# Kernel tuning notes

Measured on AMD Instinct MI355X. Metric: run time of the kernel, lower is better.

The kernel has to match this reference:

```python
import jax, jax.numpy as jnp
import numpy as np

D_MODEL = 1024
D_STATE = 16
D_CONV = 4
EXPAND = 2
HEADDIM = 8
D_INNER = EXPAND * D_MODEL            # 2048
NHEADS = D_INNER // HEADDIM           # 256
CONV_DIM = D_INNER + 2 * D_STATE      # 2080 (ngroups=1)
D_IN_PROJ = 2 * D_INNER + 2 * D_STATE + NHEADS  # 4384
B_SZ, SEQ = 4, 2048
EPS = 1e-5


def setup_inputs() -> dict:
    key = jax.random.key(0)
    ks = jax.random.split(key, 8)
    return {
        "x": jax.random.normal(ks[0], (B_SZ, SEQ, D_MODEL), jnp.float32),
        "ln_w": jnp.ones((D_MODEL,), jnp.float32),
        "ln_b": jnp.zeros((D_MODEL,), jnp.float32),
        "W_in": jax.random.normal(ks[1], (D_MODEL, D_IN_PROJ), jnp.float32) * 0.02,
        "conv_w": jax.random.normal(ks[2], (D_CONV, 1, CONV_DIM), jnp.float32) * 0.2,
        "conv_b": jnp.zeros((CONV_DIM,), jnp.float32),
        "A_log": jnp.log(jax.random.uniform(ks[3], (NHEADS,), jnp.float32, 1.0, 16.0)),
        "Dp": jnp.ones((NHEADS,), jnp.float32) + 0.1 * jax.random.normal(ks[4], (NHEADS,), jnp.float32),
        "dt_bias": 0.5 * jax.random.normal(ks[5], (NHEADS,), jnp.float32),
        "rms_w": jnp.ones((D_INNER,), jnp.float32),
        "W_out": jax.random.normal(ks[6], (D_INNER, D_MODEL), jnp.float32) * 0.02,
    }


def _mamba_block(x, ln_w, ln_b, W_in, conv_w, conv_b, A_log, Dp, dt_bias, rms_w, W_out):
    B, L, _ = x.shape
    # pre-norm LayerNorm
    mu = jnp.mean(x, axis=-1, keepdims=True)
    var = jnp.mean((x - mu) ** 2, axis=-1, keepdims=True)
    xn = (x - mu) * jax.lax.rsqrt(var + EPS) * ln_w + ln_b

    # in_proj -> z, xBC, dt
    u = xn @ W_in                                    # (B, L, 4384)
    z = u[..., :D_INNER]
    xBC = u[..., D_INNER:D_INNER + CONV_DIM]
    dt = jax.nn.softplus(u[..., -NHEADS:] + dt_bias)  # (B, L, NHEADS)

    # causal depthwise conv1d + SiLU
    xp = jnp.pad(xBC, ((0, 0), (D_CONV - 1, 0), (0, 0)))
    xBC = jax.lax.conv_general_dilated(
        xp, conv_w, window_strides=(1,), padding="VALID",
        dimension_numbers=("NWC", "WIO", "NWC"), feature_group_count=CONV_DIM)
    xBC = jax.nn.silu(xBC + conv_b)

    xs = xBC[..., :D_INNER].reshape(B, L, NHEADS, HEADDIM)   # SSM input
    Bm = xBC[..., D_INNER:D_INNER + D_STATE]                  # (B, L, N)
    Cm = xBC[..., D_INNER + D_STATE:]                          # (B, L, N)

    A = -jnp.exp(A_log)                                       # (NHEADS,)

    def step(h, inp):
        # h: (B, H, P, N)
        x_t, B_t, C_t, dt_t = inp
        dA = jnp.exp(dt_t * A)                                 # (B, H)
        h = h * dA[..., None, None] + jnp.einsum("bh,bhp,bn->bhpn", dt_t, x_t, B_t)
        y = jnp.einsum("bhpn,bn->bhp", h, C_t)
        return h, y

    h0 = jnp.zeros((B, NHEADS, HEADDIM, D_STATE), x.dtype)
    _, ys = jax.lax.scan(step, h0, (xs.swapaxes(0, 1), Bm.swapaxes(0, 1),
                                     Cm.swapaxes(0, 1), dt.swapaxes(0, 1)))
    y = ys.swapaxes(0, 1) + Dp[None, None, :, None] * xs       # (B, L, H, P)
    y = y.reshape(B, L, D_INNER)

    # gated RMSNorm: rmsnorm(y * silu(z)) * weight
    g = y * jax.nn.silu(z)
    g = g * jax.lax.rsqrt(jnp.mean(g * g, axis=-1, keepdims=True) + EPS) * rms_w

    return x + g @ W_out


def reference(x, ln_w, ln_b, W_in, conv_w, conv_b, A_log, Dp, dt_bias, rms_w, W_out):
    return _mamba_block(x, ln_w, ln_b, W_in, conv_w, conv_b, A_log, Dp, dt_bias, rms_w, W_out)
```

## Files before the change

### kernel.cpp

```cpp
#include <hip/hip_runtime.h>

typedef __bf16 bf16;
typedef __attribute__((ext_vector_type(8))) __bf16 bf16x8;
typedef __attribute__((ext_vector_type(4))) float f32x4;

#define B_SZ 4
#define SEQ 2048
#define DM 1024
#define DIN 2048
#define NH 256
#define DSTATE 16
#define CONVD 2080
#define DPROJ 4384
#define NPAD1 4608
#define MROWS 8192
#define NC 64
#define LC 32
#define UROWB 8768

__device__ __forceinline__ void gload_lds16(const void* g, void* l) {
  __builtin_amdgcn_global_load_lds(
      (__attribute__((address_space(1))) void*)g,
      (__attribute__((address_space(3))) void*)l, 16, 0, 0);
}

template <int N>
__device__ __forceinline__ void vm_wait() {
  asm volatile("s_waitcnt vmcnt(%0)" ::"n"(N) : "memory");
}
__device__ __forceinline__ void bar() { asm volatile("s_barrier" ::: "memory"); }
__device__ __forceinline__ void lgkm0() {
  asm volatile("s_waitcnt lgkmcnt(0)" ::: "memory");
}

__global__ void transpose_cvt(const float* __restrict__ W, bf16* __restrict__ WT,
                              int K, int N, int Npad) {
  __shared__ float tile[32][33];
  int k0 = blockIdx.x * 32, n0 = blockIdx.y * 32;
  int tx = threadIdx.x, ty = threadIdx.y;
#pragma unroll
  for (int j = 0; j < 4; j++) {
    int k = k0 + ty + 8 * j, n = n0 + tx;
    tile[ty + 8 * j][tx] = (k < K && n < N) ? W[(size_t)k * N + n] : 0.f;
  }
  __syncthreads();
#pragma unroll
  for (int j = 0; j < 4; j++) {
    int n = n0 + ty + 8 * j, k = k0 + tx;
    if (n < Npad && k < K) WT[(size_t)n * K + k] = (bf16)tile[tx][ty + 8 * j];
  }
}

__global__ __launch_bounds__(256) void ln_kernel(const float* __restrict__ x,
                                                 const float* __restrict__ lw,
                                                 const float* __restrict__ lb,
                                                 bf16* __restrict__ xn) {
  int row = blockIdx.x;
  int t = threadIdx.x;
  f32x4 v4 = ((const f32x4*)(x + (size_t)row * DM))[t];
  float v0 = v4[0], v1 = v4[1], v2 = v4[2], v3 = v4[3];
  float s = v0 + v1 + v2 + v3;
  float s2 = v0 * v0 + v1 * v1 + v2 * v2 + v3 * v3;
#pragma unroll
  for (int off = 32; off > 0; off >>= 1) {
    s += __shfl_down(s, off);
    s2 += __shfl_down(s2, off);
  }
  __shared__ float ps[8];
  int wave = t >> 6, lane = t & 63;
  if (lane == 0) { ps[wave] = s; ps[4 + wave] = s2; }
  __syncthreads();
  s = ps[0] + ps[1] + ps[2] + ps[3];
  s2 = ps[4] + ps[5] + ps[6] + ps[7];
  float mean = s * (1.f / DM);
  float var = s2 * (1.f / DM) - mean * mean;
  float rstd = rsqrtf(var + 1e-5f);
  f32x4 wv = ((const f32x4*)lw)[t];
  f32x4 bv = ((const f32x4*)lb)[t];
  bf16 o[4];
  o[0] = (bf16)((v0 - mean) * rstd * wv[0] + bv[0]);
  o[1] = (bf16)((v1 - mean) * rstd * wv[1] + bv[1]);
  o[2] = (bf16)((v2 - mean) * rstd * wv[2] + bv[2]);
  o[3] = (bf16)((v3 - mean) * rstd * wv[3] + bv[3]);
  bf16* dst = xn + (size_t)row * DM + t * 4;
  dst[0] = o[0]; dst[1] = o[1]; dst[2] = o[2]; dst[3] = o[3];
}

__global__ __launch_bounds__(512, 2) void gemm1_8p(const bf16* __restrict__ A,
                                                   const bf16* __restrict__ BT,
                                                   bf16* __restrict__ C) {
  __shared__ char lds[139264];
  int bid = blockIdx.x;
  int xcd = bid & 7;
  int l = bid >> 3;
  int bm = xcd * 4 + ((l >> 3) & 3);
  int bn = (l >> 5) * 8 + (l & 7);
  int m0 = bm * 256, n0 = bn * 192;
  int t = threadIdx.x, lane = t & 63, wave = t >> 6;
  int wm = wave >> 2, wn = wave & 3;
  int lr16 = lane & 15, kq = lane >> 4;
  int ts0 = kq ^ (lr16 & 7);
  int ts1 = (4 + kq) ^ (lr16 & 7);
  int sw = (lane & 7) ^ (lane >> 3);
  int l8 = lane >> 3;
  const char* Ab = (const char*)A;
  const char* Bb = (const char*)BT;

  auto stA = [&](int kt) {
    char* slot = lds + (kt & 1) * 32768;
    size_t ko = (size_t)kt * 128 + sw * 16;
#pragma unroll
    for (int g = 0; g < 4; g++) {
      int c = wave * 4 + g;
      gload_lds16(Ab + (size_t)(m0 + c * 8 + l8) * 2048 + ko, slot + c * 1024);
    }
  };
  auto stB = [&](int kt) {
    char* slot = lds + 65536 + (kt % 3) * 24576;
    size_t ko = (size_t)kt * 128 + sw * 16;
#pragma unroll
    for (int g = 0; g < 3; g++) {
      int c = wave * 3 + g;
      gload_lds16(Bb + (size_t)(n0 + c * 8 + l8) * 2048 + ko, slot + c * 1024);
    }
  };

  f32x4 acc[8][3] = {};
  bf16x8 a_[4][2], b_[3][2];

  stA(0); stB(0); stA(1); stB(1);
  vm_wait<7>();
  bar();
#pragma unroll 1
  for (int kt = 0; kt < 16; kt++) {
    {
      const char* sa = lds + (kt & 1) * 32768;
      const char* sb = lds + 65536 + (kt % 3) * 24576;
#pragma unroll
      for (int mi = 0; mi < 4; mi++) {
        int lrow = wm * 128 + mi * 16 + lr16;
        a_[mi][0] = *(const bf16x8*)(sa + lrow * 128 + ts0 * 16);
        a_[mi][1] = *(const bf16x8*)(sa + lrow * 128 + ts1 * 16);
      }
#pragma unroll
      for (int ni = 0; ni < 3; ni++) {
        int lrow = wn * 48 + ni * 16 + lr16;
        b_[ni][0] = *(const bf16x8*)(sb + lrow * 128 + ts0 * 16);
        b_[ni][1] = *(const bf16x8*)(sb + lrow * 128 + ts1 * 16);
      }
      if (kt >= 1 && kt < 15) stA(kt + 1);
      if (kt < 14) stB(kt + 2);
      bar();
      lgkm0();
      __builtin_amdgcn_s_setprio(1);
#pragma unroll
      for (int mi = 0; mi < 4; mi++)
#pragma unroll
        for (int ni = 0; ni < 3; ni++) {
          acc[mi][ni] = __builtin_amdgcn_mfma_f32_16x16x32_bf16(a_[mi][0], b_[ni][0], acc[mi][ni], 0, 0, 0);
          acc[mi][ni] = __builtin_amdgcn_mfma_f32_16x16x32_bf16(a_[mi][1], b_[ni][1], acc[mi][ni], 0, 0, 0);
        }
      __builtin_amdgcn_s_setprio(0);
      bar();
    }
    {
      const char* sa = lds + (kt & 1) * 32768;
#pragma unroll
      for (int mi = 0; mi < 4; mi++) {
        int lrow = wm * 128 + 64 + mi * 16 + lr16;
        a_[mi][0] = *(const bf16x8*)(sa + lrow * 128 + ts0 * 16);
        a_[mi][1] = *(const bf16x8*)(sa + lrow * 128 + ts1 * 16);
      }
      if (kt <= 13) vm_wait<3>();
      else if (kt == 14) vm_wait<0>();
      bar();
      lgkm0();
      __builtin_amdgcn_s_setprio(1);
#pragma unroll
      for (int mi = 0; mi < 4; mi++)
#pragma unroll
        for (int ni = 0; ni < 3; ni++) {
          acc[4 + mi][ni] = __builtin_amdgcn_mfma_f32_16x16x32_bf16(a_[mi][0], b_[ni][0], acc[4 + mi][ni], 0, 0, 0);
          acc[4 + mi][ni] = __builtin_amdgcn_mfma_f32_16x16x32_bf16(a_[mi][1], b_[ni][1], acc[4 + mi][ni], 0, 0, 0);
        }
      __builtin_amdgcn_s_setprio(0);
      bar();
    }
  }
#pragma unroll
  for (int fr = 0; fr < 8; fr++)
#pragma unroll
    for (int ni = 0; ni < 3; ni++) {
      int row = m0 + wm * 128 + fr * 16 + kq * 4;
      int col = n0 + wn * 48 + ni * 16 + lr16;
      f32x4 v = acc[fr][ni];
      if (col < 4384) {
#pragma unroll
        for (int r = 0; r < 4; r++)
          C[(size_t)(row + r) * DPROJ + col] = (bf16)v[r];
      }
    }
}

__global__ __launch_bounds__(512, 2) void gemm2_8p(const bf16* __restrict__ A,
                                                   const bf16* __restrict__ BT,
                                                   float* __restrict__ C,
                                                   const float* __restrict__ Xres) {
  __shared__ char lds[147456];
  int bid = blockIdx.x;
  int swz = (bid & 7) * 32 + (bid >> 3);
  int bm = swz >> 2, bn = swz & 3;
  int m0 = bm * 128, n0 = bn * 256;
  int t = threadIdx.x, lane = t & 63, wave = t >> 6;
  int wm = wave >> 2, wn = wave & 3;
  int lr16 = lane & 15, kq = lane >> 4;
  int ts0 = kq ^ (lr16 & 7);
  int ts1 = (4 + kq) ^ (lr16 & 7);
  int sw = (lane & 7) ^ (lane >> 3);
  int l8 = lane >> 3;
  const char* Ab = (const char*)A;
  const char* Bb = (const char*)BT;

  auto stA = [&](int kt) {
    char* slot = lds + (kt % 3) * 16384;
    size_t ko = (size_t)kt * 128 + sw * 16;
#pragma unroll
    for (int g = 0; g < 2; g++) {
      int c = wave * 2 + g;
      gload_lds16(Ab + (size_t)(m0 + c * 8 + l8) * 4096 + ko, slot + c * 1024);
    }
  };
  auto stB = [&](int kt) {
    char* slot = lds + 49152 + (kt % 3) * 32768;
    size_t ko = (size_t)kt * 128 + sw * 16;
#pragma unroll
    for (int g = 0; g < 4; g++) {
      int c = wave * 4 + g;
      gload_lds16(Bb + (size_t)(n0 + c * 8 + l8) * 4096 + ko, slot + c * 1024);
    }
  };

  f32x4 acc[4][4] = {};
  bf16x8 a_[4][2], b_[2][2];

  stA(0); stB(0); stA(1); stB(1);
  vm_wait<6>();
  bar();
#pragma unroll 1
  for (int kt = 0; kt < 32; kt++) {
    const char* sa = lds + (kt % 3) * 16384;
    const char* sb = lds + 49152 + (kt % 3) * 32768;
    {
#pragma unroll
      for (int mi = 0; mi < 4; mi++) {
        int lrow = wm * 64 + mi * 16 + lr16;
        a_[mi][0] = *(const bf16x8*)(sa + lrow * 128 + ts0 * 16);
        a_[mi][1] = *(const bf16x8*)(sa + lrow * 128 + ts1 * 16);
      }
#pragma unroll
      for (int ni = 0; ni < 2; ni++) {
        int lrow = wn * 64 + ni * 16 + lr16;
        b_[ni][0] = *(const bf16x8*)(sb + lrow * 128 + ts0 * 16);
        b_[ni][1] = *(const bf16x8*)(sb + lrow * 128 + ts1 * 16);
      }
      if (kt + 2 < 32) { stA(kt + 2); stB(kt + 2); }
      bar();
      lgkm0();
      __builtin_amdgcn_s_setprio(1);
#pragma unroll
      for (int mi = 0; mi < 4; mi++)
#pragma unroll
        for (int ni = 0; ni < 2; ni++) {
          acc[mi][ni] = __builtin_amdgcn_mfma_f32_16x16x32_bf16(a_[mi][0], b_[ni][0], acc[mi][ni], 0, 0, 0);
          acc[mi][ni] = __builtin_amdgcn_mfma_f32_16x16x32_bf16(a_[mi][1], b_[ni][1], acc[mi][ni], 0, 0, 0);
        }
      __builtin_amdgcn_s_setprio(0);
      bar();
    }
    {
#pragma unroll
      for (int ni = 0; ni < 2; ni++) {
        int lrow = wn * 64 + (2 + ni) * 16 + lr16;
        b_[ni][0] = *(const bf16x8*)(sb + lrow * 128 + ts0 * 16);
        b_[ni][1] = *(const bf16x8*)(sb + lrow * 128 + ts1 * 16);
      }
      if (kt <= 29) vm_wait<6>();
      else if (kt == 30) vm_wait<0>();
      bar();
      lgkm0();
      __builtin_amdgcn_s_setprio(1);
#pragma unroll
      for (int mi = 0; mi < 4; mi++)
#pragma unroll
        for (int ni = 0; ni < 2; ni++) {
          acc[mi][2 + ni] = __builtin_amdgcn_mfma_f32_16x16x32_bf16(a_[mi][0], b_[ni][0], acc[mi][2 + ni], 0, 0, 0);
          acc[mi][2 + ni] = __builtin_amdgcn_mfma_f32_16x16x32_bf16(a_[mi][1], b_[ni][1], acc[mi][2 + ni], 0, 0, 0);
        }
      __builtin_amdgcn_s_setprio(0);
      bar();
    }
  }
#pragma unroll
  for (int mi = 0; mi < 4; mi++)
#pragma unroll
    for (int ni = 0; ni < 4; ni++) {
      int row = m0 + wm * 64 + mi * 16 + kq * 4;
      int col = n0 + wn * 64 + ni * 16 + lr16;
      f32x4 v = acc[mi][ni];
#pragma unroll
      for (int r = 0; r < 4; r++) {
        size_t o = (size_t)(row + r) * DM + col;
        C[o] = Xres[o] + v[r];
      }
    }
}

__global__ __launch_bounds__(256) void conv_prep3(const bf16* __restrict__ u,
                                                  const float* __restrict__ cw,
                                                  const float* __restrict__ cb,
                                                  const float* __restrict__ dt_bias,
                                                  bf16* __restrict__ xs,
                                                  float* __restrict__ BC,
                                                  float* __restrict__ dtf) {
  const int JPR = 292;
  int idx = blockIdx.x * 256 + threadIdx.x;
  if (idx >= MROWS * JPR) return;
  int row = idx / JPR;
  int j = idx - row * JPR;
  int t = row & (SEQ - 1);
  if (j < 260) {
    int c0 = j * 8;
    float acc[8];
#pragma unroll
    for (int i = 0; i < 8; i++) acc[i] = cb[c0 + i];
    const bf16* ub = u + (size_t)row * DPROJ + DIN + c0;
#pragma unroll
    for (int tap = 0; tap < 4; tap++) {
      int tt = t - 3 + tap;
      if (tt >= 0) {
        bf16x8 uv = *(const bf16x8*)(ub + (ptrdiff_t)(tap - 3) * DPROJ);
        const float* wv = cw + tap * CONVD + c0;
#pragma unroll
        for (int i = 0; i < 8; i++) acc[i] += wv[i] * (float)uv[i];
      }
    }
    if (c0 < DIN) {
      bf16x8 o;
#pragma unroll
      for (int i = 0; i < 8; i++) {
        float sv = acc[i] / (1.f + __expf(-acc[i]));
        o[i] = (bf16)sv;
      }
      *(bf16x8*)(xs + (size_t)row * DIN + c0) = o;
    } else {
      float* bc = BC + (size_t)row * 32 + (c0 - DIN);
#pragma unroll
      for (int i = 0; i < 8; i++) bc[i] = acc[i] / (1.f + __expf(-acc[i]));
    }
  } else {
    int h0 = (j - 260) * 8;
    bf16x8 uv = *(const bf16x8*)(u + (size_t)row * DPROJ + (DPROJ - NH) + h0);
    float* dst = dtf + (size_t)row * NH + h0;
#pragma unroll
    for (int i = 0; i < 8; i++) {
      float xv = (float)uv[i] + dt_bias[h0 + i];
      dst[i] = (xv > 20.f) ? xv : log1pf(__expf(xv));
    }
  }
}

__global__ __launch_bounds__(64) void scan_p1(const bf16* __restrict__ xs,
                                              const float* __restrict__ BC,
                                              const float* __restrict__ dtf,
                                              const float* __restrict__ A_log,
                                              bf16* __restrict__ uscr) {
  int c = blockIdx.x & 63, hg = (blockIdx.x >> 6) & 31, b = blockIdx.x >> 11;
  int lane = threadIdx.x, hh = lane >> 3;
  int h = hg * 8 + hh;
  float A = -__expf(A_log[h]);
  float st[16];
#pragma unroll
  for (int n = 0; n < 16; n++) st[n] = 0.f;
  float pcum = 1.f;
  size_t rb = (size_t)b * SEQ + (size_t)c * LC;
  for (int t = 0; t < LC; t++) {
    size_t row = rb + t;
    const float* bcrow = BC + row * 32;
    float dtv = dtf[row * NH + h];
    float x = (float)xs[row * DIN + hg * 64 + lane];
    float dA = __expf(dtv * A);
    pcum *= dA;
    float w = dtv * x;
#pragma unroll
    for (int n = 0; n < 16; n++) st[n] = st[n] * dA + w * bcrow[n];
  }
  char* slot = (char*)uscr + (size_t)blockIdx.x * UROWB + 4096;
  float* S = (float*)slot;
#pragma unroll
  for (int n = 0; n < 16; n++) S[lane * 16 + n] = st[n];
  if ((lane & 7) == 0) ((float*)(slot + 4096))[hh] = pcum;
}

__global__ __launch_bounds__(64) void scan_p2(bf16* __restrict__ uscr) {
  int bh = blockIdx.x;
  int lane = threadIdx.x, hh = lane >> 3;
  float H[16];
#pragma unroll
  for (int n = 0; n < 16; n++) H[n] = 0.f;
  char* base = (char*)uscr + (size_t)bh * NC * UROWB + 4096;
  float sN[16], PN;
  {
    float* S = (float*)base;
#pragma unroll
    for (int n = 0; n < 16; n++) sN[n] = S[lane * 16 + n];
    PN = ((const float*)(base + 4096))[hh];
  }
  for (int c = 0; c < NC; c++) {
    float sC[16], PC = PN;
#pragma unroll
    for (int n = 0; n < 16; n++) sC[n] = sN[n];
    if (c + 1 < NC) {
      char* slot = base + (size_t)(c + 1) * UROWB;
      float* S = (float*)slot;
#pragma unroll
      for (int n = 0; n < 16; n++) sN[n] = S[lane * 16 + n];
      PN = ((const float*)(slot + 4096))[hh];
    }
    float* S0 = (float*)(base + (size_t)c * UROWB);
#pragma unroll
    for (int n = 0; n < 16; n++) {
      float hn = H[n];
      S0[lane * 16 + n] = hn;
      H[n] = PC * hn + sC[n];
    }
  }
}

__global__ __launch_bounds__(64) void scan_p3(const bf16* __restrict__ xs,
                                              const float* __restrict__ BC,
                                              const float* __restrict__ dtf,
                                              const float* __restrict__ A_log,
                                              const float* __restrict__ Dp,
                                              const bf16* __restrict__ uscr,
                                              bf16* __restrict__ y) {
  int c = blockIdx.x & 63, hg = (blockIdx.x >> 6) & 31, b = blockIdx.x >> 11;
  int lane = threadIdx.x, hh = lane >> 3;
  int h = hg * 8 + hh;
  float A = -__expf(A_log[h]);
  float D = Dp[h];
  const char* slot = (const char*)uscr + (size_t)blockIdx.x * UROWB + 4096;
  float st[16];
#pragma unroll
  for (int n = 0; n < 16; n++) st[n] = ((const float*)slot)[lane * 16 + n];
  size_t rb = (size_t)b * SEQ + (size_t)c * LC;
  for (int t = 0; t < LC; t++) {
    size_t row = rb + t;
    const float* bcrow = BC + row * 32;
    float dtv = dtf[row * NH + h];
    float x = (float)xs[row * DIN + hg * 64 + lane];
    float dA = __expf(dtv * A);
    float w = dtv * x;
    float yv = 0.f;
#pragma unroll
    for (int n = 0; n < 16; n++) {
      st[n] = st[n] * dA + w * bcrow[n];
      yv += st[n] * bcrow[16 + n];
    }
    y[row * DIN + hg * 64 + lane] = (bf16)(yv + D * x);
  }
}

__global__ __launch_bounds__(256) void gate_rms(const bf16* __restrict__ u,
                                                const bf16* __restrict__ y,
                                                const float* __restrict__ rms_w,
                                                bf16* __restrict__ g) {
  int row = blockIdx.x;
  int t = threadIdx.x;
  bf16x8 zv = ((const bf16x8*)(u + (size_t)row * DPROJ))[t];
  bf16x8 yv = ((const bf16x8*)(y + (size_t)row * DIN))[t];
  float gv[8];
  float s2 = 0.f;
#pragma unroll
  for (int i = 0; i < 8; i++) {
    float z = (float)zv[i];
    float yy = (float)yv[i];
    float gg = yy * z / (1.f + __expf(-z));
    gv[i] = gg;
    s2 += gg * gg;
  }
#pragma unroll
  for (int off = 32; off > 0; off >>= 1) s2 += __shfl_down(s2, off);
  __shared__ float ps[4];
  int wave = t >> 6, lane = t & 63;
  if (lane == 0) ps[wave] = s2;
  __syncthreads();
  s2 = ps[0] + ps[1] + ps[2] + ps[3];
  float scale = rsqrtf(s2 * (1.f / DIN) + 1e-5f);
  f32x4 w0 = ((const f32x4*)rms_w)[2 * t];
  f32x4 w1 = ((const f32x4*)rms_w)[2 * t + 1];
  bf16x8 og;
#pragma unroll
  for (int i = 0; i < 4; i++) og[i] = (bf16)(gv[i] * scale * w0[i]);
#pragma unroll
  for (int i = 0; i < 4; i++) og[4 + i] = (bf16)(gv[4 + i] * scale * w1[i]);
  ((bf16x8*)(g + (size_t)row * DIN))[t] = og;
}

extern "C" void kernel_launch(void* const* d_in, const int* in_sizes, int n_in,
                              void* d_out, int out_size, void* d_ws, size_t ws_size,
                              hipStream_t stream) {
  const float* x = (const float*)d_in[0];
  const float* lnw = (const float*)d_in[1];
  const float* lnb = (const float*)d_in[2];
  const float* Win = (const float*)d_in[3];
  const float* cw = (const float*)d_in[4];
  const float* cb = (const float*)d_in[5];
  const float* Alog = (const float*)d_in[6];
  const float* Dpv = (const float*)d_in[7];
  const float* dtb = (const float*)d_in[8];
  const float* rmsw = (const float*)d_in[9];
  const float* Wout = (const float*)d_in[10];
  float* out = (float*)d_out;

  char* ws = (char*)d_ws;
  bf16* u = (bf16*)(ws + 0);
  bf16* xnb = (bf16*)(ws + 71827456);
  bf16* WinT = (bf16*)(ws + 88604672);
  bf16* yb = (bf16*)(ws + 71827456);
  bf16* xsb = (bf16*)(ws + 105381888);
  bf16* gb = (bf16*)(ws + 105381888);
  float* BC = (float*)(ws + 138936320);
  float* dtf = (float*)(ws + 139984896);
  bf16* WoutT = (bf16*)(ws + 148373504);

  transpose_cvt<<<dim3(32, 144), dim3(32, 8), 0, stream>>>(Win, WinT, 1024, DPROJ, NPAD1);
  transpose_cvt<<<dim3(64, 32), dim3(32, 8), 0, stream>>>(Wout, WoutT, DIN, DM, DM);
  ln_kernel<<<MROWS, 256, 0, stream>>>(x, lnw, lnb, xnb);
  gemm1_8p<<<768, 512, 0, stream>>>(xnb, WinT, u);
  conv_prep3<<<(MROWS * 292) / 256, 256, 0, stream>>>(u, cw, cb, dtb, xsb, BC, dtf);
  scan_p1<<<MROWS, 64, 0, stream>>>(xsb, BC, dtf, Alog, u);
  scan_p2<<<128, 64, 0, stream>>>(u);
  scan_p3<<<MROWS, 64, 0, stream>>>(xsb, BC, dtf, Alog, Dpv, u, yb);
  gate_rms<<<MROWS, 256, 0, stream>>>(u, yb, rmsw, gb);
  gemm2_8p<<<256, 512, 0, stream>>>(gb, WoutT, out, x);
}
```

Before: 296.8 us.

## Switch both GEMMs from 16x16x32 to 32x32x16 MFMA tiles

```diff
diff --git a/kernel.cpp b/kernel.cpp
--- a/kernel.cpp
+++ b/kernel.cpp
@@ -3,6 +3,7 @@
 typedef __bf16 bf16;
 typedef __attribute__((ext_vector_type(8))) __bf16 bf16x8;
 typedef __attribute__((ext_vector_type(4))) float f32x4;
+typedef __attribute__((ext_vector_type(16))) float f32x16;
 
 #define B_SZ 4
 #define SEQ 2048
@@ -97,10 +98,8 @@
   int bn = (l >> 5) * 8 + (l & 7);
   int m0 = bm * 256, n0 = bn * 192;
   int t = threadIdx.x, lane = t & 63, wave = t >> 6;
-  int wm = wave >> 2, wn = wave & 3;
-  int lr16 = lane & 15, kq = lane >> 4;
-  int ts0 = kq ^ (lr16 & 7);
-  int ts1 = (4 + kq) ^ (lr16 & 7);
+  int wm = wave >> 1, wn = wave & 1;
+  int l31 = lane & 31, kq = lane >> 5;
   int sw = (lane & 7) ^ (lane >> 3);
   int l8 = lane >> 3;
   const char* Ab = (const char*)A;
@@ -125,28 +124,31 @@
     }
   };
 
-  f32x4 acc[8][3] = {};
-  bf16x8 a_[4][2], b_[3][2];
+  f32x16 acc[2][3] = {};
+  bf16x8 a_[2][2], b_[3][2];
+  int x7 = l31 & 7;
 
   stA(0); stB(0); stA(1); stB(1);
   vm_wait<7>();
   bar();
 #pragma unroll 1
   for (int kt = 0; kt < 16; kt++) {
+    const char* sa = lds + (kt & 1) * 32768;
+    const char* sb = lds + 65536 + (kt % 3) * 24576;
     {
-      const char* sa = lds + (kt & 1) * 32768;
-      const char* sb = lds + 65536 + (kt % 3) * 24576;
-#pragma unroll
-      for (int mi = 0; mi < 4; mi++) {
-        int lrow = wm * 128 + mi * 16 + lr16;
-        a_[mi][0] = *(const bf16x8*)(sa + lrow * 128 + ts0 * 16);
-        a_[mi][1] = *(const bf16x8*)(sa + lrow * 128 + ts1 * 16);
+#pragma unroll
+      for (int mi = 0; mi < 2; mi++) {
+        int row = wm * 64 + mi * 32 + l31;
+#pragma unroll
+        for (int s = 0; s < 2; s++)
+          a_[mi][s] = *(const bf16x8*)(sa + row * 128 + ((s * 2 + kq) ^ x7) * 16);
       }
 #pragma unroll
       for (int ni = 0; ni < 3; ni++) {
-        int lrow = wn * 48 + ni * 16 + lr16;
-        b_[ni][0] = *(const bf16x8*)(sb + lrow * 128 + ts0 * 16);
-        b_[ni][1] = *(const bf16x8*)(sb + lrow * 128 + ts1 * 16);
+        int row = wn * 96 + ni * 32 + l31;
+#pragma unroll
+        for (int s = 0; s < 2; s++)
+          b_[ni][s] = *(const bf16x8*)(sb + row * 128 + ((s * 2 + kq) ^ x7) * 16);
       }
       if (kt >= 1 && kt < 15) stA(kt + 1);
       if (kt < 14) stB(kt + 2);
@@ -154,22 +156,29 @@
       lgkm0();
       __builtin_amdgcn_s_setprio(1);
 #pragma unroll
-      for (int mi = 0; mi < 4; mi++)
-#pragma unroll
-        for (int ni = 0; ni < 3; ni++) {
-          acc[mi][ni] = __builtin_amdgcn_mfma_f32_16x16x32_bf16(a_[mi][0], b_[ni][0], acc[mi][ni], 0, 0, 0);
-          acc[mi][ni] = __builtin_amdgcn_mfma_f32_16x16x32_bf16(a_[mi][1], b_[ni][1], acc[mi][ni], 0, 0, 0);
-        }
+      for (int s = 0; s < 2; s++)
+#pragma unroll
+        for (int mi = 0; mi < 2; mi++)
+#pragma unroll
+          for (int ni = 0; ni < 3; ni++)
+            acc[mi][ni] = __builtin_amdgcn_mfma_f32_32x32x16_bf16(a_[mi][s], b_[ni][s], acc[mi][ni], 0, 0, 0);
       __builtin_amdgcn_s_setprio(0);
       bar();
     }
     {
-      const char* sa = lds + (kt & 1) * 32768;
-#pragma unroll
-      for (int mi = 0; mi < 4; mi++) {
-        int lrow = wm * 128 + 64 + mi * 16 + lr16;
-        a_[mi][0] = *(const bf16x8*)(sa + lrow * 128 + ts0 * 16);
-        a_[mi][1] = *(const bf16x8*)(sa + lrow * 128 + ts1 * 16);
+#pragma unroll
+      for (int mi = 0; mi < 2; mi++) {
+        int row = wm * 64 + mi * 32 + l31;
+#pragma unroll
+        for (int s = 0; s < 2; s++)
+          a_[mi][s] = *(const bf16x8*)(sa + row * 128 + (((2 + s) * 2 + kq) ^ x7) * 16);
+      }
+#pragma unroll
+      for (int ni = 0; ni < 3; ni++) {
+        int row = wn * 96 + ni * 32 + l31;
+#pragma unroll
+        for (int s = 0; s < 2; s++)
+          b_[ni][s] = *(const bf16x8*)(sb + row * 128 + (((2 + s) * 2 + kq) ^ x7) * 16);
       }
       if (kt <= 13) vm_wait<3>();
       else if (kt == 14) vm_wait<0>();
@@ -177,27 +186,29 @@
       lgkm0();
       __builtin_amdgcn_s_setprio(1);
 #pragma unroll
-      for (int mi = 0; mi < 4; mi++)
-#pragma unroll
-        for (int ni = 0; ni < 3; ni++) {
-          acc[4 + mi][ni] = __builtin_amdgcn_mfma_f32_16x16x32_bf16(a_[mi][0], b_[ni][0], acc[4 + mi][ni], 0, 0, 0);
-          acc[4 + mi][ni] = __builtin_amdgcn_mfma_f32_16x16x32_bf16(a_[mi][1], b_[ni][1], acc[4 + mi][ni], 0, 0, 0);
+      for (int s = 0; s < 2; s++)
+#pragma unroll
+        for (int mi = 0; mi < 2; mi++)
+#pragma unroll
+          for (int ni = 0; ni < 3; ni++)
+            acc[mi][ni] = __builtin_amdgcn_mfma_f32_32x32x16_bf16(a_[mi][s], b_[ni][s], acc[mi][ni], 0, 0, 0);
+      __builtin_amdgcn_s_setprio(0);
+      bar();
+    }
+  }
+#pragma unroll
+  for (int mi = 0; mi < 2; mi++)
+#pragma unroll
+    for (int ni = 0; ni < 3; ni++) {
+      int r0 = m0 + wm * 64 + mi * 32 + 4 * kq;
+      int col = n0 + wn * 96 + ni * 32 + l31;
+      f32x16 v = acc[mi][ni];
+      if (col < 4384) {
+#pragma unroll
+        for (int r = 0; r < 16; r++) {
+          int row = r0 + (r & 3) + 8 * (r >> 2);
+          C[(size_t)row * DPROJ + col] = (bf16)v[r];
         }
-      __builtin_amdgcn_s_setprio(0);
-      bar();
-    }
-  }
-#pragma unroll
-  for (int fr = 0; fr < 8; fr++)
-#pragma unroll
-    for (int ni = 0; ni < 3; ni++) {
-      int row = m0 + wm * 128 + fr * 16 + kq * 4;
-      int col = n0 + wn * 48 + ni * 16 + lr16;
-      f32x4 v = acc[fr][ni];
-      if (col < 4384) {
-#pragma unroll
-        for (int r = 0; r < 4; r++)
-          C[(size_t)(row + r) * DPROJ + col] = (bf16)v[r];
       }
     }
 }
@@ -213,11 +224,10 @@
   int m0 = bm * 128, n0 = bn * 256;
   int t = threadIdx.x, lane = t & 63, wave = t >> 6;
   int wm = wave >> 2, wn = wave & 3;
-  int lr16 = lane & 15, kq = lane >> 4;
-  int ts0 = kq ^ (lr16 & 7);
-  int ts1 = (4 + kq) ^ (lr16 & 7);
+  int l31 = lane & 31, kq = lane >> 5;
   int sw = (lane & 7) ^ (lane >> 3);
   int l8 = lane >> 3;
+  int x7 = l31 & 7;
   const char* Ab = (const char*)A;
   const char* Bb = (const char*)BT;
 
@@ -240,8 +250,8 @@
     }
   };
 
-  f32x4 acc[4][4] = {};
-  bf16x8 a_[4][2], b_[2][2];
+  f32x16 acc[2][2] = {};
+  bf16x8 a_[2][2], b_[2][2];
 
   stA(0); stB(0); stA(1); stB(1);
   vm_wait<6>();
@@ -252,37 +262,47 @@
     const char* sb = lds + 49152 + (kt % 3) * 32768;
     {
 #pragma unroll
-      for (int mi = 0; mi < 4; mi++) {
-        int lrow = wm * 64 + mi * 16 + lr16;
-        a_[mi][0] = *(const bf16x8*)(sa + lrow * 128 + ts0 * 16);
-        a_[mi][1] = *(const bf16x8*)(sa + lrow * 128 + ts1 * 16);
+      for (int mi = 0; mi < 2; mi++) {
+        int row = wm * 64 + mi * 32 + l31;
+#pragma unroll
+        for (int s = 0; s < 2; s++)
+          a_[mi][s] = *(const bf16x8*)(sa + row * 128 + ((s * 2 + kq) ^ x7) * 16);
       }
 #pragma unroll
       for (int ni = 0; ni < 2; ni++) {
-        int lrow = wn * 64 + ni * 16 + lr16;
-        b_[ni][0] = *(const bf16x8*)(sb + lrow * 128 + ts0 * 16);
-        b_[ni][1] = *(const bf16x8*)(sb + lrow * 128 + ts1 * 16);
+        int row = wn * 64 + ni * 32 + l31;
+#pragma unroll
+        for (int s = 0; s < 2; s++)
+          b_[ni][s] = *(const bf16x8*)(sb + row * 128 + ((s * 2 + kq) ^ x7) * 16);
       }
       if (kt + 2 < 32) { stA(kt + 2); stB(kt + 2); }
       bar();
       lgkm0();
       __builtin_amdgcn_s_setprio(1);
 #pragma unroll
-      for (int mi = 0; mi < 4; mi++)
-#pragma unroll
-        for (int ni = 0; ni < 2; ni++) {
-          acc[mi][ni] = __builtin_amdgcn_mfma_f32_16x16x32_bf16(a_[mi][0], b_[ni][0], acc[mi][ni], 0, 0, 0);
-          acc[mi][ni] = __builtin_amdgcn_mfma_f32_16x16x32_bf16(a_[mi][1], b_[ni][1], acc[mi][ni], 0, 0, 0);
-        }
+      for (int s = 0; s < 2; s++)
+#pragma unroll
+        for (int mi = 0; mi < 2; mi++)
+#pragma unroll
+          for (int ni = 0; ni < 2; ni++)
+            acc[mi][ni] = __builtin_amdgcn_mfma_f32_32x32x16_bf16(a_[mi][s], b_[ni][s], acc[mi][ni], 0, 0, 0);
       __builtin_amdgcn_s_setprio(0);
       bar();
     }
     {
 #pragma unroll
+      for (int mi = 0; mi < 2; mi++) {
+        int row = wm * 64 + mi * 32 + l31;
+#pragma unroll
+        for (int s = 0; s < 2; s++)
+          a_[mi][s] = *(const bf16x8*)(sa + row * 128 + (((2 + s) * 2 + kq) ^ x7) * 16);
+      }
+#pragma unroll
       for (int ni = 0; ni < 2; ni++) {
-        int lrow = wn * 64 + (2 + ni) * 16 + lr16;
-        b_[ni][0] = *(const bf16x8*)(sb + lrow * 128 + ts0 * 16);
-        b_[ni][1] = *(const bf16x8*)(sb + lrow * 128 + ts1 * 16);
+        int row = wn * 64 + ni * 32 + l31;
+#pragma unroll
+        for (int s = 0; s < 2; s++)
+          b_[ni][s] = *(const bf16x8*)(sb + row * 128 + (((2 + s) * 2 + kq) ^ x7) * 16);
       }
       if (kt <= 29) vm_wait<6>();
       else if (kt == 30) vm_wait<0>();
@@ -290,26 +310,27 @@
       lgkm0();
       __builtin_amdgcn_s_setprio(1);
 #pragma unroll
-      for (int mi = 0; mi < 4; mi++)
-#pragma unroll
-        for (int ni = 0; ni < 2; ni++) {
-          acc[mi][2 + ni] = __builtin_amdgcn_mfma_f32_16x16x32_bf16(a_[mi][0], b_[ni][0], acc[mi][2 + ni], 0, 0, 0);
-          acc[mi][2 + ni] = __builtin_amdgcn_mfma_f32_16x16x32_bf16(a_[mi][1], b_[ni][1], acc[mi][2 + ni], 0, 0, 0);
-        }
+      for (int s = 0; s < 2; s++)
+#pragma unroll
+        for (int mi = 0; mi < 2; mi++)
+#pragma unroll
+          for (int ni = 0; ni < 2; ni++)
+            acc[mi][ni] = __builtin_amdgcn_mfma_f32_32x32x16_bf16(a_[mi][s], b_[ni][s], acc[mi][ni], 0, 0, 0);
       __builtin_amdgcn_s_setprio(0);
       bar();
     }
   }
 #pragma unroll
-  for (int mi = 0; mi < 4; mi++)
-#pragma unroll
-    for (int ni = 0; ni < 4; ni++) {
-      int row = m0 + wm * 64 + mi * 16 + kq * 4;
-      int col = n0 + wn * 64 + ni * 16 + lr16;
-      f32x4 v = acc[mi][ni];
-#pragma unroll
-      for (int r = 0; r < 4; r++) {
-        size_t o = (size_t)(row + r) * DM + col;
+  for (int mi = 0; mi < 2; mi++)
+#pragma unroll
+    for (int ni = 0; ni < 2; ni++) {
+      int r0 = m0 + wm * 64 + mi * 32 + 4 * kq;
+      int col = n0 + wn * 64 + ni * 32 + l31;
+      f32x16 v = acc[mi][ni];
+#pragma unroll
+      for (int r = 0; r < 16; r++) {
+        int row = r0 + (r & 3) + 8 * (r >> 2);
+        size_t o = (size_t)row * DM + col;
         C[o] = Xres[o] + v[r];
       }
     }
```

Measured after the change: 300.3 us. About the same (+1.2%).
